# Performance work log

Measured on AMD Instinct MI355X. Metric: run time of the kernel, lower is better.

The kernel has to match this reference:

```python
import jax, jax.numpy as jnp
import numpy as np

B, T, H = 32, 4096, 256

def setup_inputs() -> dict:
    key = jax.random.key(0)
    k1, k2, k3, k4, k5 = jax.random.split(key, 5)
    hidden = jax.random.normal(k1, (B, H), dtype=jnp.float32)
    encoder_outputs = jax.random.normal(k2, (T, B, H), dtype=jnp.float32)
    # nn.Linear(2H, H): weight [H, 2H], bias [H] (kaiming-uniform-ish scale)
    bound = 1.0 / np.sqrt(2 * H)
    attn_w = jax.random.uniform(k3, (H, 2 * H), minval=-bound, maxval=bound, dtype=jnp.float32)
    attn_b = jax.random.uniform(k4, (H,), minval=-bound, maxval=bound, dtype=jnp.float32)
    v = jax.random.uniform(k5, (H,), dtype=jnp.float32)  # torch.rand -> U[0,1)
    return {"hidden": hidden, "encoder_outputs": encoder_outputs,
            "attn_w": attn_w, "attn_b": attn_b, "v": v}

def reference(hidden, encoder_outputs, attn_w, attn_b, v):
    # hidden: [B, H]; encoder_outputs: [T, B, H]
    t = encoder_outputs.shape[0]
    enc = jnp.transpose(encoder_outputs, (1, 0, 2))            # [B, T, H]
    h = jnp.broadcast_to(hidden[:, None, :], enc.shape)        # [B, T, H]
    temp = jnp.concatenate([h, enc], axis=2)                   # [B, T, 2H]
    energy = jax.nn.relu(jnp.einsum('btk,hk->bth', temp, attn_w) + attn_b)  # [B, T, H]
    scores = jnp.einsum('bth,h->bt', energy, v)                # [B, T]
    return jax.nn.softmax(scores, axis=1)[:, None, :]          # [B, 1, T]
```

## Files before the change

kernel.cpp:

```cpp
#include <hip/hip_runtime.h>
#include <hip/hip_bf16.h>

#define B_SZ 32
#define T_SZ 4096
#define H_SZ 256
#define M_SZ (T_SZ * B_SZ)
#define SROW 72

typedef __attribute__((ext_vector_type(8))) short bf16x8;
typedef __attribute__((ext_vector_type(4))) short bf16x4;
typedef __attribute__((ext_vector_type(4))) float f32x4;

static __device__ __forceinline__ short f2bf(float x) {
    unsigned u = __float_as_uint(x);
    u += 0x7fffu + ((u >> 16) & 1u);
    return (short)(u >> 16);
}

static __device__ __forceinline__ bf16x4 cvt4(f32x4 a) {
    bf16x4 r;
    r[0] = f2bf(a[0]); r[1] = f2bf(a[1]); r[2] = f2bf(a[2]); r[3] = f2bf(a[3]);
    return r;
}

__global__ __launch_bounds__(256) void prep_kernel(
    const float* __restrict__ hidden, const float* __restrict__ attn_w,
    const float* __restrict__ attn_b, float* __restrict__ hpT,
    short* __restrict__ wbf2)
{
    const int h   = blockIdx.x;
    const int tid = threadIdx.x;
    __shared__ float wsh[H_SZ];

    wsh[tid] = attn_w[(size_t)h * 512 + tid];
    {
        const int k = tid;
        const int hs = h >> 6, nt = (h >> 4) & 3, r = h & 15;
        const int s = k >> 5, quad = (k >> 3) & 3, e = k & 7;
        wbf2[(hs * 4 + nt) * 4096 + s * 512 + quad * 128 + r * 8 + e] =
            f2bf(attn_w[(size_t)h * 512 + 256 + k]);
    }
    __syncthreads();

    const int b  = tid >> 3;
    const int kg = tid & 7;
    const float* hrow = hidden + b * H_SZ + kg * 32;
    const float* wrow = wsh + kg * 32;
    float s = 0.f;
#pragma unroll
    for (int j = 0; j < 32; j += 4) {
        f32x4 hv = *(const f32x4*)(hrow + j);
        s = fmaf(hv[0], wrow[j + 0], s);
        s = fmaf(hv[1], wrow[j + 1], s);
        s = fmaf(hv[2], wrow[j + 2], s);
        s = fmaf(hv[3], wrow[j + 3], s);
    }
#pragma unroll
    for (int off = 1; off < 8; off <<= 1) s += __shfl_xor(s, off, 8);
    if (kg == 0) hpT[h * B_SZ + b] = s + attn_b[h];
}

__global__ __launch_bounds__(256, 2) void attn_main(
    const float* __restrict__ enc,
    const short* __restrict__ wbf2,
    const float* __restrict__ hpT,
    const float* __restrict__ v,
    float* __restrict__ scores)
{
    __shared__ __align__(16) short As[2][64 * SROW];
    __shared__ float part[4][64];

    const int blk  = blockIdx.x;
    const int m0   = blk << 6;
    const int tid  = threadIdx.x;
    const int w    = tid >> 6;
    const int lane = tid & 63;
    const int r    = lane & 15;
    const int quad = lane >> 4;
    const int hbase = w * 64;

    const int sr  = tid >> 4;
    const int sc4 = (tid & 15) * 4;
    const float* sp = enc + (size_t)(m0 + sr) * H_SZ + sc4;
    short* sdB[2];
    sdB[0] = &As[0][0] + sr * SROW + sc4;
    sdB[1] = &As[1][0] + sr * SROW + sc4;

    const short* wp = wbf2 + (size_t)w * 16384 + lane * 8;

    f32x4 g[4][4];
#pragma unroll
    for (int kc = 0; kc < 4; ++kc)
#pragma unroll
        for (int i = 0; i < 4; ++i)
            g[kc][i] = *(const f32x4*)(sp + i * 16 * H_SZ + kc * 64);

    bf16x8 bc[2][4];
#pragma unroll
    for (int ss = 0; ss < 2; ++ss)
#pragma unroll
        for (int nt = 0; nt < 4; ++nt)
            bc[ss][nt] = *(const bf16x8*)(wp + nt * 4096 + ss * 512);

    f32x4 acc[4][4];
#pragma unroll
    for (int mt = 0; mt < 4; ++mt)
#pragma unroll
        for (int nt = 0; nt < 4; ++nt)
            acc[mt][nt] = (f32x4){0.f, 0.f, 0.f, 0.f};

#pragma unroll
    for (int i = 0; i < 4; ++i)
        *(bf16x4*)(sdB[0] + i * 16 * SROW) = cvt4(g[0][i]);
    __syncthreads();

#pragma unroll
    for (int kc = 0; kc < 4; ++kc) {
        const short* abase = &As[kc & 1][0] + quad * 8;
#pragma unroll
        for (int ss = 0; ss < 2; ++ss) {
            bf16x8 af[4];
#pragma unroll
            for (int mt = 0; mt < 4; ++mt)
                af[mt] = *(const bf16x8*)(abase + (mt * 16 + r) * SROW + ss * 32);
#pragma unroll
            for (int mt = 0; mt < 4; ++mt)
#pragma unroll
                for (int nt = 0; nt < 4; ++nt)
                    acc[mt][nt] = __builtin_amdgcn_mfma_f32_16x16x32_bf16(
                        af[mt], bc[ss][nt], acc[mt][nt], 0, 0, 0);
        }

        if (kc < 3) {
            const int ko = (kc + 1) * 2;
#pragma unroll
            for (int ss = 0; ss < 2; ++ss)
#pragma unroll
                for (int nt = 0; nt < 4; ++nt)
                    bc[ss][nt] = *(const bf16x8*)(wp + nt * 4096 + (ko + ss) * 512);

            short* d = sdB[(kc + 1) & 1];
#pragma unroll
            for (int i = 0; i < 4; ++i)
                *(bf16x4*)(d + i * 16 * SROW) = cvt4(g[kc + 1][i]);
            __syncthreads();
        }
    }

    float vv[4];
    f32x4 hpv[2][4];
#pragma unroll
    for (int nt = 0; nt < 4; ++nt) {
        const int h = hbase + nt * 16 + r;
        vv[nt] = v[h];
        hpv[0][nt] = *(const f32x4*)(hpT + h * B_SZ + quad * 4);
        hpv[1][nt] = *(const f32x4*)(hpT + h * B_SZ + 16 + quad * 4);
    }

#pragma unroll
    for (int mt = 0; mt < 4; ++mt) {
#pragma unroll
        for (int reg = 0; reg < 4; ++reg) {
            float s = 0.f;
#pragma unroll
            for (int nt = 0; nt < 4; ++nt) {
                float e = hpv[mt & 1][nt][reg] + acc[mt][nt][reg];
                e = fmaxf(e, 0.f);
                s = fmaf(vv[nt], e, s);
            }
#pragma unroll
            for (int off = 1; off < 16; off <<= 1) s += __shfl_xor(s, off, 16);
            if (r == 0) part[w][mt * 16 + quad * 4 + reg] = s;
        }
    }
    __syncthreads();
    if (tid < 64) {
        float sc = part[0][tid] + part[1][tid] + part[2][tid] + part[3][tid];
        const int b = tid & 31;
        const int t = (m0 + tid) >> 5;
        scores[b * T_SZ + t] = sc;
    }
}

__global__ __launch_bounds__(1024) void softmax_kernel(
    const float* __restrict__ scores, float* __restrict__ out)
{
    const int b   = blockIdx.x;
    const int tid = threadIdx.x;
    const float* s = scores + b * T_SZ;
    float*       o = out    + b * T_SZ;

    float loc[4];
    float m = -3.0e38f;
#pragma unroll
    for (int i = 0; i < 4; ++i) {
        loc[i] = s[tid + i * 1024];
        m = fmaxf(m, loc[i]);
    }
    __shared__ float redm[16], reds[16];
#pragma unroll
    for (int off = 32; off > 0; off >>= 1) m = fmaxf(m, __shfl_xor(m, off, 64));
    if ((tid & 63) == 0) redm[tid >> 6] = m;
    __syncthreads();
#pragma unroll
    for (int i = 0; i < 16; ++i) m = fmaxf(m, redm[i]);

    float sum = 0.f;
#pragma unroll
    for (int i = 0; i < 4; ++i) {
        loc[i] = __expf(loc[i] - m);
        sum += loc[i];
    }
#pragma unroll
    for (int off = 32; off > 0; off >>= 1) sum += __shfl_xor(sum, off, 64);
    if ((tid & 63) == 0) reds[tid >> 6] = sum;
    __syncthreads();
    sum = 0.f;
#pragma unroll
    for (int i = 0; i < 16; ++i) sum += reds[i];
    const float inv = 1.0f / sum;
#pragma unroll
    for (int i = 0; i < 4; ++i) o[tid + i * 1024] = loc[i] * inv;
}

extern "C" void kernel_launch(void* const* d_in, const int* in_sizes, int n_in,
                              void* d_out, int out_size, void* d_ws, size_t ws_size,
                              hipStream_t stream) {
    const float* hidden = (const float*)d_in[0];
    const float* enc    = (const float*)d_in[1];
    const float* attn_w = (const float*)d_in[2];
    const float* attn_b = (const float*)d_in[3];
    const float* v      = (const float*)d_in[4];
    float* out = (float*)d_out;

    float* hpT    = (float*)d_ws;
    float* scores = hpT + H_SZ * B_SZ;
    short* wbf2   = (short*)(scores + B_SZ * T_SZ);

    hipLaunchKernelGGL(prep_kernel, dim3(H_SZ), dim3(256), 0, stream,
                       hidden, attn_w, attn_b, hpT, wbf2);
    hipLaunchKernelGGL(attn_main, dim3(M_SZ / 64), dim3(256), 0, stream,
                       enc, wbf2, hpT, v, scores);
    hipLaunchKernelGGL(softmax_kernel, dim3(B_SZ), dim3(1024), 0, stream,
                       scores, out);
}
```

Measured before the change: 218.6 us.

## Load encoder tile via direct global-to-LDS DMA and halve block M-tile

The main kernel now copies the fp32 encoder rows straight into shared memory with global_load_lds, instead of staging them through registers and converting to bf16 before the LDS store. The bf16 conversion moves to after the LDS read. The block tile shrinks from 64 to 32 rows, the grid doubles, and launch bounds raise occupancy to 4 blocks per CU. The intent is to cut register pressure and VGPR staging and to let more blocks hide memory latency. In exchange, W fragments are reloaded from global memory by twice as many blocks, and the fp32 LDS reads and conversions land on the MFMA critical path.

```diff
diff --git a/kernel.cpp b/kernel.cpp
--- a/kernel.cpp
+++ b/kernel.cpp
@@ -5,10 +5,9 @@
 #define T_SZ 4096
 #define H_SZ 256
 #define M_SZ (T_SZ * B_SZ)
-#define SROW 72
+#define AROW 260
 
 typedef __attribute__((ext_vector_type(8))) short bf16x8;
-typedef __attribute__((ext_vector_type(4))) short bf16x4;
 typedef __attribute__((ext_vector_type(4))) float f32x4;
 
 static __device__ __forceinline__ short f2bf(float x) {
@@ -17,10 +16,18 @@
     return (short)(u >> 16);
 }
 
-static __device__ __forceinline__ bf16x4 cvt4(f32x4 a) {
-    bf16x4 r;
+static __device__ __forceinline__ bf16x8 cvt8(f32x4 a, f32x4 b) {
+    bf16x8 r;
     r[0] = f2bf(a[0]); r[1] = f2bf(a[1]); r[2] = f2bf(a[2]); r[3] = f2bf(a[3]);
+    r[4] = f2bf(b[0]); r[5] = f2bf(b[1]); r[6] = f2bf(b[2]); r[7] = f2bf(b[3]);
     return r;
+}
+
+static __device__ __forceinline__ void dma16(const float* g, const uint32_t* l) {
+    __builtin_amdgcn_global_load_lds(
+        (const __attribute__((address_space(1))) void*)(uintptr_t)g,
+        (__attribute__((address_space(3))) void*)(uintptr_t)l,
+        16, 0, 0);
 }
 
 __global__ __launch_bounds__(256) void prep_kernel(
@@ -60,18 +67,18 @@
     if (kg == 0) hpT[h * B_SZ + b] = s + attn_b[h];
 }
 
-__global__ __launch_bounds__(256, 2) void attn_main(
+__global__ __launch_bounds__(256, 4) void attn_main(
     const float* __restrict__ enc,
     const short* __restrict__ wbf2,
     const float* __restrict__ hpT,
     const float* __restrict__ v,
     float* __restrict__ scores)
 {
-    __shared__ __align__(16) short As[2][64 * SROW];
-    __shared__ float part[4][64];
+    __shared__ __align__(16) uint32_t At[32 * AROW];
+    __shared__ float part[4][32];
 
     const int blk  = blockIdx.x;
-    const int m0   = blk << 6;
+    const int m0   = blk << 5;
     const int tid  = threadIdx.x;
     const int w    = tid >> 6;
     const int lane = tid & 63;
@@ -79,72 +86,55 @@
     const int quad = lane >> 4;
     const int hbase = w * 64;
 
-    const int sr  = tid >> 4;
-    const int sc4 = (tid & 15) * 4;
-    const float* sp = enc + (size_t)(m0 + sr) * H_SZ + sc4;
-    short* sdB[2];
-    sdB[0] = &As[0][0] + sr * SROW + sc4;
-    sdB[1] = &As[1][0] + sr * SROW + sc4;
+    const float* gbase = enc + (size_t)(m0 + 8 * w) * H_SZ + lane * 4;
+    const uint32_t* lbase = At + (8 * w) * AROW;
+#pragma unroll
+    for (int i = 0; i < 8; ++i)
+        dma16(gbase + i * H_SZ, lbase + i * AROW);
 
     const short* wp = wbf2 + (size_t)w * 16384 + lane * 8;
 
-    f32x4 g[4][4];
-#pragma unroll
-    for (int kc = 0; kc < 4; ++kc)
-#pragma unroll
-        for (int i = 0; i < 4; ++i)
-            g[kc][i] = *(const f32x4*)(sp + i * 16 * H_SZ + kc * 64);
-
-    bf16x8 bc[2][4];
-#pragma unroll
-    for (int ss = 0; ss < 2; ++ss)
-#pragma unroll
-        for (int nt = 0; nt < 4; ++nt)
-            bc[ss][nt] = *(const bf16x8*)(wp + nt * 4096 + ss * 512);
-
-    f32x4 acc[4][4];
-#pragma unroll
-    for (int mt = 0; mt < 4; ++mt)
+    bf16x8 bc[4];
+#pragma unroll
+    for (int nt = 0; nt < 4; ++nt)
+        bc[nt] = *(const bf16x8*)(wp + nt * 4096);
+
+    f32x4 acc[2][4];
+#pragma unroll
+    for (int mt = 0; mt < 2; ++mt)
 #pragma unroll
         for (int nt = 0; nt < 4; ++nt)
             acc[mt][nt] = (f32x4){0.f, 0.f, 0.f, 0.f};
 
-#pragma unroll
-    for (int i = 0; i < 4; ++i)
-        *(bf16x4*)(sdB[0] + i * 16 * SROW) = cvt4(g[0][i]);
-    __syncthreads();
-
-#pragma unroll
-    for (int kc = 0; kc < 4; ++kc) {
-        const short* abase = &As[kc & 1][0] + quad * 8;
-#pragma unroll
-        for (int ss = 0; ss < 2; ++ss) {
-            bf16x8 af[4];
-#pragma unroll
-            for (int mt = 0; mt < 4; ++mt)
-                af[mt] = *(const bf16x8*)(abase + (mt * 16 + r) * SROW + ss * 32);
-#pragma unroll
-            for (int mt = 0; mt < 4; ++mt)
-#pragma unroll
-                for (int nt = 0; nt < 4; ++nt)
-                    acc[mt][nt] = __builtin_amdgcn_mfma_f32_16x16x32_bf16(
-                        af[mt], bc[ss][nt], acc[mt][nt], 0, 0, 0);
+    __syncthreads();
+
+#pragma unroll
+    for (int kc = 0; kc < 8; ++kc) {
+        bf16x8 bn[4];
+        if (kc < 7) {
+#pragma unroll
+            for (int nt = 0; nt < 4; ++nt)
+                bn[nt] = *(const bf16x8*)(wp + nt * 4096 + (kc + 1) * 512);
         }
 
-        if (kc < 3) {
-            const int ko = (kc + 1) * 2;
-#pragma unroll
-            for (int ss = 0; ss < 2; ++ss)
-#pragma unroll
-                for (int nt = 0; nt < 4; ++nt)
-                    bc[ss][nt] = *(const bf16x8*)(wp + nt * 4096 + (ko + ss) * 512);
-
-            short* d = sdB[(kc + 1) & 1];
-#pragma unroll
-            for (int i = 0; i < 4; ++i)
-                *(bf16x4*)(d + i * 16 * SROW) = cvt4(g[kc + 1][i]);
-            __syncthreads();
+        bf16x8 af[2];
+#pragma unroll
+        for (int mt = 0; mt < 2; ++mt) {
+            const uint32_t* a = At + (mt * 16 + r) * AROW + kc * 32 + quad * 8;
+            f32x4 lo = *(const f32x4*)a;
+            f32x4 hi = *(const f32x4*)(a + 4);
+            af[mt] = cvt8(lo, hi);
         }
+
+#pragma unroll
+        for (int mt = 0; mt < 2; ++mt)
+#pragma unroll
+            for (int nt = 0; nt < 4; ++nt)
+                acc[mt][nt] = __builtin_amdgcn_mfma_f32_16x16x32_bf16(
+                    af[mt], bc[nt], acc[mt][nt], 0, 0, 0);
+
+#pragma unroll
+        for (int nt = 0; nt < 4; ++nt) bc[nt] = bn[nt];
     }
 
     float vv[4];
@@ -158,13 +148,13 @@
     }
 
 #pragma unroll
-    for (int mt = 0; mt < 4; ++mt) {
+    for (int mt = 0; mt < 2; ++mt) {
 #pragma unroll
         for (int reg = 0; reg < 4; ++reg) {
             float s = 0.f;
 #pragma unroll
             for (int nt = 0; nt < 4; ++nt) {
-                float e = hpv[mt & 1][nt][reg] + acc[mt][nt][reg];
+                float e = hpv[mt][nt][reg] + acc[mt][nt][reg];
                 e = fmaxf(e, 0.f);
                 s = fmaf(vv[nt], e, s);
             }
@@ -174,9 +164,9 @@
         }
     }
     __syncthreads();
-    if (tid < 64) {
+    if (tid < 32) {
         float sc = part[0][tid] + part[1][tid] + part[2][tid] + part[3][tid];
-        const int b = tid & 31;
+        const int b = tid;
         const int t = (m0 + tid) >> 5;
         scores[b * T_SZ + t] = sc;
     }
@@ -239,7 +229,7 @@
 
     hipLaunchKernelGGL(prep_kernel, dim3(H_SZ), dim3(256), 0, stream,
                        hidden, attn_w, attn_b, hpT, wbf2);
-    hipLaunchKernelGGL(attn_main, dim3(M_SZ / 64), dim3(256), 0, stream,
+    hipLaunchKernelGGL(attn_main, dim3(M_SZ / 32), dim3(256), 0, stream,
                        enc, wbf2, hpT, v, scores);
     hipLaunchKernelGGL(softmax_kernel, dim3(B_SZ), dim3(1024), 0, stream,
                        scores, out);
```

After: 227.4 us. +4.0%, slower.
